# Performance work log

Hardware: AMD Instinct MI355X
Metric: run time of the kernel (lower is better)

## Reference

```python
import jax, jax.numpy as jnp
import numpy as np

D = 128

def setup_inputs() -> dict:
    key = jax.random.key(0)
    k1, k2, k3, k4, k5, k6, k7 = jax.random.split(key, 7)
    B, L = 2048, 200
    target = jax.random.normal(k1, (B, D), dtype=jnp.float32)
    item_seq = jax.random.normal(k2, (B, L, D), dtype=jnp.float32)
    seq_len = jax.random.randint(k3, (B,), 0, 200, dtype=jnp.int64 if jax.config.jax_enable_x64 else jnp.int32)
    # MLP params: Linear(4D -> 2D), Linear(2D -> 1), PyTorch-style init scale
    s1 = 1.0 / np.sqrt(4 * D)
    s2 = 1.0 / np.sqrt(2 * D)
    W1 = jax.random.uniform(k4, (4 * D, 2 * D), minval=-s1, maxval=s1, dtype=jnp.float32)
    b1 = jax.random.uniform(k5, (2 * D,), minval=-s1, maxval=s1, dtype=jnp.float32)
    W2 = jax.random.uniform(k6, (2 * D, 1), minval=-s2, maxval=s2, dtype=jnp.float32)
    b2 = jax.random.uniform(k7, (1,), minval=-s2, maxval=s2, dtype=jnp.float32)
    return {"target": target, "item_seq": item_seq, "seq_len": seq_len,
            "W1": W1, "b1": b1, "W2": W2, "b2": b2}

def reference(target, item_seq, seq_len, W1, b1, W2, b2):
    B, L, Dd = item_seq.shape
    t = target[:, None, :]                              # B 1 D (broadcast over L)
    tgt = jnp.broadcast_to(t, (B, L, Dd))
    sub = item_seq - tgt
    dot = item_seq * tgt
    mlp_in = jnp.concatenate([tgt, item_seq, sub, dot], axis=-1)   # B L 4D
    h = jax.nn.relu(jnp.einsum('blf,fh->blh', mlp_in, W1) + b1)    # B L 2D
    score = jnp.einsum('blh,ho->blo', h, W2) + b2                  # B L 1
    mask = (jnp.arange(L)[None, :] < seq_len[:, None]).astype(item_seq.dtype)  # B L
    weighted = score * item_seq * mask[:, :, None]                 # B L D
    return jnp.sum(weighted, axis=1)                               # B D
```

## Files before the change

### kernel.cpp

```cpp
#include <hip/hip_runtime.h>
#include <hip/hip_bf16.h>

typedef short short8 __attribute__((ext_vector_type(8)));
typedef float f32x4 __attribute__((ext_vector_type(4)));

#define XS 136

static __device__ inline short f2bf(float f) {
    unsigned u = __float_as_uint(f);
    unsigned r = (u + 0x7fffu + ((u >> 16) & 1u)) >> 16;
    return (short)r;
}
static __device__ inline float bf2f(short s) {
    return __uint_as_float(((unsigned)(unsigned short)s) << 16);
}
static __device__ inline unsigned cvtpk(float lo, float hi) {
    unsigned r;
    asm("v_cvt_pk_bf16_f32 %0, %1, %2" : "=v"(r) : "v"(lo), "v"(hi));
    return r;
}

__global__ void precompute(const float* __restrict__ W1, const float* __restrict__ b1,
                           const float* __restrict__ target, short* __restrict__ Wbc,
                           short* __restrict__ Wd, float* __restrict__ U) {
    __shared__ float tl[1024];
    const int tid = threadIdx.x;
    if (blockIdx.x >= 256) {
        int idx = (blockIdx.x - 256) * 256 + tid;
        int half = idx >> 15;
        int i = idx & 32767;
        int j = i & 7;
        int l = (i >> 3) & 63;
        int s = (i >> 9) & 3;
        int t = i >> 11;
        int k = s * 32 + ((l >> 4) << 3) + j;
        int n = t * 16 + (l & 15);
        if (half == 0) Wbc[i] = f2bf(W1[(128 + k) * 256 + n] + W1[(256 + k) * 256 + n]);
        else           Wd[i]  = f2bf(W1[(384 + k) * 256 + n]);
        return;
    }
    const int b8 = blockIdx.x;
#pragma unroll
    for (int k = 0; k < 4; k++) tl[k * 256 + tid] = target[b8 * 1024 + k * 256 + tid];
    __syncthreads();
    float acc[8] = {0.f, 0.f, 0.f, 0.f, 0.f, 0.f, 0.f, 0.f};
#pragma unroll 8
    for (int d = 0; d < 128; ++d) {
        float wud = W1[d * 256 + tid] - W1[(256 + d) * 256 + tid];
#pragma unroll
        for (int r = 0; r < 8; r++) acc[r] += tl[r * 128 + d] * wud;
    }
    float bj = b1[tid];
#pragma unroll
    for (int r = 0; r < 8; r++) U[(b8 * 8 + r) * 256 + tid] = acc[r] + bj;
}

__launch_bounds__(256, 2)
__global__ void din_main(const float* __restrict__ target, const float* __restrict__ item_seq,
                         const int* __restrict__ seq_len, const float* __restrict__ W2,
                         const float* __restrict__ b2p, const short* __restrict__ Wbc,
                         const short* __restrict__ Wd, const float* __restrict__ U,
                         float* __restrict__ out) {
    const int b = blockIdx.x;
    const int tid = threadIdx.x;
    const int lane = tid & 63;
    const int w = tid >> 6;
    const int col = lane & 15;
    const int q = lane >> 4;

    const int slen = seq_len[b];
    const int nt = (slen + 15) >> 4;

    if (nt == 0) {
        if (tid < 128) out[b * 128 + tid] = 0.f;
        return;
    }

    __shared__ __attribute__((aligned(16))) short Xl[4][16 * XS];
    __shared__ __attribute__((aligned(16))) float scoreP[2][16][4];
    __shared__ __attribute__((aligned(16))) float outr[8][128];

    const int r = tid >> 4;
    const int c = (tid & 15) << 3;

    const float* item_b = item_seq + ((size_t)b * 200 + r) * 128 + c;

    float4 v0, v1;
    {
        const float4* src = (const float4*)item_b;
        v0 = src[0]; v1 = src[1];
    }

    const float b2 = b2p[0];

    float u_c[4], w2c[4];
#pragma unroll
    for (int i = 0; i < 4; i++) {
        int j = (w * 4 + i) * 16 + col;
        u_c[i] = U[b * 256 + j];
        w2c[i] = W2[j];
    }

    short8 bfrag[4][4];
    const float* tgt = target + b * 128;
#pragma unroll
    for (int s = 0; s < 4; s++) {
        const float4* tp = (const float4*)(tgt + s * 32 + q * 8);
        float4 ta = tp[0], tb = tp[1];
        float tk[8] = {ta.x, ta.y, ta.z, ta.w, tb.x, tb.y, tb.z, tb.w};
#pragma unroll
        for (int i = 0; i < 4; i++) {
            size_t off = ((size_t)((w * 4 + i) * 4 + s) * 64 + lane) * 8;
            short8 bc = *(const short8*)(Wbc + off);
            short8 dd = *(const short8*)(Wd + off);
            float f0 = fmaf(tk[0], bf2f(dd[0]), bf2f(bc[0]));
            float f1 = fmaf(tk[1], bf2f(dd[1]), bf2f(bc[1]));
            float f2 = fmaf(tk[2], bf2f(dd[2]), bf2f(bc[2]));
            float f3 = fmaf(tk[3], bf2f(dd[3]), bf2f(bc[3]));
            float f4 = fmaf(tk[4], bf2f(dd[4]), bf2f(bc[4]));
            float f5 = fmaf(tk[5], bf2f(dd[5]), bf2f(bc[5]));
            float f6 = fmaf(tk[6], bf2f(dd[6]), bf2f(bc[6]));
            float f7 = fmaf(tk[7], bf2f(dd[7]), bf2f(bc[7]));
            uint4 pe;
            pe.x = cvtpk(f0, f1);
            pe.y = cvtpk(f2, f3);
            pe.z = cvtpk(f4, f5);
            pe.w = cvtpk(f6, f7);
            bfrag[i][s] = *(short8*)&pe;
        }
    }

    const int qd = tid & 31;
    const int gg = tid >> 5;
    f32x4 ov = (f32x4){0.f, 0.f, 0.f, 0.f};

    auto accum_tile = [&](int pt) {
        const short* xp = Xl[pt & 3];
        const int l0p = pt * 16;
#pragma unroll
        for (int rr = 0; rr < 2; rr++) {
            int m = gg * 2 + rr;
            float4 sp = *(const float4*)&scoreP[pt & 1][m][0];
            float s = (sp.x + sp.y) + (sp.z + sp.w) + b2;
            s = (l0p + m < slen) ? s : 0.f;
            uint2 xv = *(const uint2*)(xp + m * XS + 4 * qd);
            float x0 = __uint_as_float(xv.x << 16);
            float x1 = __uint_as_float(xv.x & 0xffff0000u);
            float x2 = __uint_as_float(xv.y << 16);
            float x3 = __uint_as_float(xv.y & 0xffff0000u);
            ov[0] = fmaf(s, x0, ov[0]);
            ov[1] = fmaf(s, x1, ov[1]);
            ov[2] = fmaf(s, x2, ov[2]);
            ov[3] = fmaf(s, x3, ov[3]);
        }
    };

    for (int mt = 0; mt < nt; ++mt) {
        short* xb = Xl[mt & 3];

        {
            uint4 pk;
            pk.x = cvtpk(v0.x, v0.y);
            pk.y = cvtpk(v0.z, v0.w);
            pk.z = cvtpk(v1.x, v1.y);
            pk.w = cvtpk(v1.z, v1.w);
            *(uint4*)(xb + r * XS + c) = pk;
        }
        __syncthreads();

        if (mt + 1 < nt) {
            int lr = (mt + 1) * 16 + r;
            if (lr > 199) lr = 199;
            const float4* src = (const float4*)(item_b + ((size_t)(lr - r)) * 128);
            v0 = src[0]; v1 = src[1];
        }

        f32x4 acc[4];
#pragma unroll
        for (int i = 0; i < 4; i++) acc[i] = (f32x4){u_c[i], u_c[i], u_c[i], u_c[i]};
        const short* arow = xb + col * XS + q * 8;
#pragma unroll
        for (int s = 0; s < 4; s++) {
            short8 af = *(const short8*)(arow + s * 32);
#pragma unroll
            for (int i = 0; i < 4; i++)
                acc[i] = __builtin_amdgcn_mfma_f32_16x16x32_bf16(af, bfrag[i][s], acc[i], 0, 0, 0);
        }

        float sv[4];
#pragma unroll
        for (int rg = 0; rg < 4; rg++) {
            float s0 = 0.f;
#pragma unroll
            for (int i = 0; i < 4; i++) {
                float h = acc[i][rg];
                h = h > 0.f ? h : 0.f;
                s0 = fmaf(h, w2c[i], s0);
            }
            sv[rg] = s0;
        }
#pragma unroll
        for (int off = 1; off < 16; off <<= 1) {
#pragma unroll
            for (int rg = 0; rg < 4; rg++) sv[rg] += __shfl_xor(sv[rg], off, 64);
        }
        if (col == 0) {
#pragma unroll
            for (int rg = 0; rg < 4; rg++) scoreP[mt & 1][q * 4 + rg][w] = sv[rg];
        }

        if (mt > 0) accum_tile(mt - 1);
    }

    __syncthreads();
    accum_tile(nt - 1);

    *(float4*)&outr[gg][4 * qd] = *(float4*)&ov;
    __syncthreads();
    if (tid < 128) {
        float s = 0.f;
#pragma unroll
        for (int k = 0; k < 8; k++) s += outr[k][tid];
        out[b * 128 + tid] = s;
    }
}

extern "C" void kernel_launch(void* const* d_in, const int* in_sizes, int n_in,
                              void* d_out, int out_size, void* d_ws, size_t ws_size,
                              hipStream_t stream) {
    const float* target   = (const float*)d_in[0];
    const float* item_seq = (const float*)d_in[1];
    const int*   seq_len  = (const int*)d_in[2];
    const float* W1       = (const float*)d_in[3];
    const float* b1       = (const float*)d_in[4];
    const float* W2       = (const float*)d_in[5];
    const float* b2       = (const float*)d_in[6];
    float* out = (float*)d_out;

    char* ws = (char*)d_ws;
    short* Wbc = (short*)ws;
    short* Wd  = (short*)(ws + 65536);
    float* U   = (float*)(ws + 131072);

    precompute<<<512, 256, 0, stream>>>(W1, b1, target, Wbc, Wd, U);
    din_main<<<2048, 256, 0, stream>>>(target, item_seq, seq_len, W2, b2, Wbc, Wd, U, out);
}
```

Measured before the change: 298.2 us.

## Split main kernel work across 512 threads with two column groups per wave

Doubles the block to 8 waves so each wave computes two 16-column MFMA groups instead of four, and each thread loads one float4 of the item tile instead of two. Score partials and output reduction buffers widen to match the extra waves, and launch bounds request more resident blocks. The aim is to cut per-thread register pressure and serial MFMA work and to raise the number of memory requests in flight. The cost is more barrier participants and a wider final reduction.

New measurement: 311.1 us. +4.3%, slower.

```diff
diff --git a/kernel.cpp b/kernel.cpp
--- a/kernel.cpp
+++ b/kernel.cpp
@@ -55,7 +55,7 @@
     for (int r = 0; r < 8; r++) U[(b8 * 8 + r) * 256 + tid] = acc[r] + bj;
 }
 
-__launch_bounds__(256, 2)
+__launch_bounds__(512, 4)
 __global__ void din_main(const float* __restrict__ target, const float* __restrict__ item_seq,
                          const int* __restrict__ seq_len, const float* __restrict__ W2,
                          const float* __restrict__ b2p, const short* __restrict__ Wbc,
@@ -77,31 +77,27 @@
     }
 
     __shared__ __attribute__((aligned(16))) short Xl[4][16 * XS];
-    __shared__ __attribute__((aligned(16))) float scoreP[2][16][4];
-    __shared__ __attribute__((aligned(16))) float outr[8][128];
-
-    const int r = tid >> 4;
-    const int c = (tid & 15) << 3;
-
-    const float* item_b = item_seq + ((size_t)b * 200 + r) * 128 + c;
-
-    float4 v0, v1;
-    {
-        const float4* src = (const float4*)item_b;
-        v0 = src[0]; v1 = src[1];
-    }
+    __shared__ __attribute__((aligned(16))) float scoreP[2][16][8];
+    __shared__ __attribute__((aligned(16))) float outr[16][128];
+
+    const int r = tid >> 5;
+    const int cq = tid & 31;
+
+    const float* item_b = item_seq + ((size_t)b * 200 + r) * 128 + cq * 4;
+
+    float4 v0 = *(const float4*)item_b;
 
     const float b2 = b2p[0];
 
-    float u_c[4], w2c[4];
-#pragma unroll
-    for (int i = 0; i < 4; i++) {
-        int j = (w * 4 + i) * 16 + col;
+    float u_c[2], w2c[2];
+#pragma unroll
+    for (int i = 0; i < 2; i++) {
+        int j = (w * 2 + i) * 16 + col;
         u_c[i] = U[b * 256 + j];
         w2c[i] = W2[j];
     }
 
-    short8 bfrag[4][4];
+    short8 bfrag[2][4];
     const float* tgt = target + b * 128;
 #pragma unroll
     for (int s = 0; s < 4; s++) {
@@ -109,8 +105,8 @@
         float4 ta = tp[0], tb = tp[1];
         float tk[8] = {ta.x, ta.y, ta.z, ta.w, tb.x, tb.y, tb.z, tb.w};
 #pragma unroll
-        for (int i = 0; i < 4; i++) {
-            size_t off = ((size_t)((w * 4 + i) * 4 + s) * 64 + lane) * 8;
+        for (int i = 0; i < 2; i++) {
+            size_t off = ((size_t)((w * 2 + i) * 4 + s) * 64 + lane) * 8;
             short8 bc = *(const short8*)(Wbc + off);
             short8 dd = *(const short8*)(Wd + off);
             float f0 = fmaf(tk[0], bf2f(dd[0]), bf2f(bc[0]));
@@ -130,74 +126,54 @@
         }
     }
 
-    const int qd = tid & 31;
-    const int gg = tid >> 5;
     f32x4 ov = (f32x4){0.f, 0.f, 0.f, 0.f};
 
     auto accum_tile = [&](int pt) {
         const short* xp = Xl[pt & 3];
-        const int l0p = pt * 16;
-#pragma unroll
-        for (int rr = 0; rr < 2; rr++) {
-            int m = gg * 2 + rr;
-            float4 sp = *(const float4*)&scoreP[pt & 1][m][0];
-            float s = (sp.x + sp.y) + (sp.z + sp.w) + b2;
-            s = (l0p + m < slen) ? s : 0.f;
-            uint2 xv = *(const uint2*)(xp + m * XS + 4 * qd);
-            float x0 = __uint_as_float(xv.x << 16);
-            float x1 = __uint_as_float(xv.x & 0xffff0000u);
-            float x2 = __uint_as_float(xv.y << 16);
-            float x3 = __uint_as_float(xv.y & 0xffff0000u);
-            ov[0] = fmaf(s, x0, ov[0]);
-            ov[1] = fmaf(s, x1, ov[1]);
-            ov[2] = fmaf(s, x2, ov[2]);
-            ov[3] = fmaf(s, x3, ov[3]);
-        }
+        const float4* sp4 = (const float4*)&scoreP[pt & 1][r][0];
+        float4 sa = sp4[0], sb = sp4[1];
+        float s = ((sa.x + sa.y) + (sa.z + sa.w)) + ((sb.x + sb.y) + (sb.z + sb.w)) + b2;
+        s = (pt * 16 + r < slen) ? s : 0.f;
+        uint2 xv = *(const uint2*)(xp + r * XS + 4 * cq);
+        ov[0] = fmaf(s, __uint_as_float(xv.x << 16), ov[0]);
+        ov[1] = fmaf(s, __uint_as_float(xv.x & 0xffff0000u), ov[1]);
+        ov[2] = fmaf(s, __uint_as_float(xv.y << 16), ov[2]);
+        ov[3] = fmaf(s, __uint_as_float(xv.y & 0xffff0000u), ov[3]);
     };
 
     for (int mt = 0; mt < nt; ++mt) {
         short* xb = Xl[mt & 3];
 
         {
-            uint4 pk;
+            uint2 pk;
             pk.x = cvtpk(v0.x, v0.y);
             pk.y = cvtpk(v0.z, v0.w);
-            pk.z = cvtpk(v1.x, v1.y);
-            pk.w = cvtpk(v1.z, v1.w);
-            *(uint4*)(xb + r * XS + c) = pk;
+            *(uint2*)(xb + r * XS + 4 * cq) = pk;
         }
         __syncthreads();
 
         if (mt + 1 < nt) {
             int lr = (mt + 1) * 16 + r;
             if (lr > 199) lr = 199;
-            const float4* src = (const float4*)(item_b + ((size_t)(lr - r)) * 128);
-            v0 = src[0]; v1 = src[1];
-        }
-
-        f32x4 acc[4];
-#pragma unroll
-        for (int i = 0; i < 4; i++) acc[i] = (f32x4){u_c[i], u_c[i], u_c[i], u_c[i]};
+            v0 = *(const float4*)(item_b + ((size_t)(lr - r)) * 128);
+        }
+
+        f32x4 acc0 = (f32x4){u_c[0], u_c[0], u_c[0], u_c[0]};
+        f32x4 acc1 = (f32x4){u_c[1], u_c[1], u_c[1], u_c[1]};
         const short* arow = xb + col * XS + q * 8;
 #pragma unroll
         for (int s = 0; s < 4; s++) {
             short8 af = *(const short8*)(arow + s * 32);
-#pragma unroll
-            for (int i = 0; i < 4; i++)
-                acc[i] = __builtin_amdgcn_mfma_f32_16x16x32_bf16(af, bfrag[i][s], acc[i], 0, 0, 0);
+            acc0 = __builtin_amdgcn_mfma_f32_16x16x32_bf16(af, bfrag[0][s], acc0, 0, 0, 0);
+            acc1 = __builtin_amdgcn_mfma_f32_16x16x32_bf16(af, bfrag[1][s], acc1, 0, 0, 0);
         }
 
         float sv[4];
 #pragma unroll
         for (int rg = 0; rg < 4; rg++) {
-            float s0 = 0.f;
-#pragma unroll
-            for (int i = 0; i < 4; i++) {
-                float h = acc[i][rg];
-                h = h > 0.f ? h : 0.f;
-                s0 = fmaf(h, w2c[i], s0);
-            }
-            sv[rg] = s0;
+            float h0 = acc0[rg] > 0.f ? acc0[rg] : 0.f;
+            float h1 = acc1[rg] > 0.f ? acc1[rg] : 0.f;
+            sv[rg] = fmaf(h0, w2c[0], h1 * w2c[1]);
         }
 #pragma unroll
         for (int off = 1; off < 16; off <<= 1) {
@@ -215,12 +191,12 @@
     __syncthreads();
     accum_tile(nt - 1);
 
-    *(float4*)&outr[gg][4 * qd] = *(float4*)&ov;
+    *(float4*)&outr[r][4 * cq] = *(float4*)&ov;
     __syncthreads();
     if (tid < 128) {
         float s = 0.f;
 #pragma unroll
-        for (int k = 0; k < 8; k++) s += outr[k][tid];
+        for (int k = 0; k < 16; k++) s += outr[k][tid];
         out[b * 128 + tid] = s;
     }
 }
@@ -243,5 +219,5 @@
     float* U   = (float*)(ws + 131072);
 
     precompute<<<512, 256, 0, stream>>>(W1, b1, target, Wbc, Wd, U);
-    din_main<<<2048, 256, 0, stream>>>(target, item_seq, seq_len, W2, b2, Wbc, Wd, U, out);
-}
+    din_main<<<2048, 512, 0, stream>>>(target, item_seq, seq_len, W2, b2, Wbc, Wd, U, out);
+}
```
